# Performance work log

Hardware: AMD Instinct MI355X
Metric: run time of the kernel (lower is better)

The kernel has to match this reference:

```python
import jax, jax.numpy as jnp
import numpy as np
from jax import lax

TAU = 30.0  # softmax temperature


def setup_inputs() -> dict:
    key = jax.random.key(0)
    ks = jax.random.split(key, 6)
    N, Ci, Co, H, K, KW = 16, 64, 64, 256, 3, 4
    x = jax.random.normal(ks[0], (N, Ci, H, H), jnp.float32)
    # bank of KW candidate kernels: (Co, KW, Ci, K, K), kaiming-ish scale
    w_bank = jax.random.normal(ks[1], (Co, KW, Ci, K, K), jnp.float32) * (2.0 / (Co * K * K)) ** 0.5
    b_bank = jax.random.normal(ks[2], (Co, KW), jnp.float32) * 0.01
    # attention MLP (two 1x1 convs): Ci -> Ci//KW -> KW
    att_w1 = jax.random.normal(ks[3], (Ci // KW, Ci), jnp.float32) * (1.0 / Ci) ** 0.5
    att_b1 = jnp.zeros((Ci // KW,), jnp.float32)
    att_w2 = jax.random.normal(ks[4], (KW, Ci // KW), jnp.float32) * (KW / Ci) ** 0.5
    att_b2 = jnp.zeros((KW,), jnp.float32)
    return {"x": x, "w_bank": w_bank, "b_bank": b_bank,
            "att_w1": att_w1, "att_b1": att_b1, "att_w2": att_w2, "att_b2": att_b2}


def reference(x, w_bank, b_bank, att_w1, att_b1, att_w2, att_b2):
    # attention over weight banks: 1x1 conv -> ReLU -> 1x1 conv -> global avg pool -> softmax(/tau)
    h = jax.nn.relu(jnp.einsum('nchw,dc->ndhw', x, att_w1) + att_b1[None, :, None, None])
    logits = jnp.einsum('ndhw,ed->nehw', h, att_w2) + att_b2[None, :, None, None]
    pooled = jnp.mean(logits, axis=(2, 3))          # [N, KW] (avg_pool2d with kernel=H on square input)
    pi = jax.nn.softmax(pooled / TAU, axis=1)       # [N, KW]
    # per-sample aggregated kernels/biases
    w = jnp.einsum('okcij,nk->nocij', w_bank, pi)   # [N, Co, Ci, K, K]
    b = jnp.einsum('ok,nk->no', b_bank, pi)         # [N, Co]
    # per-sample conv (equivalent to the groups=N conv2d trick)
    def conv_one(xi, wi):
        return lax.conv_general_dilated(xi[None], wi, window_strides=(1, 1),
                                        padding=[(1, 1), (1, 1)],
                                        dimension_numbers=('NCHW', 'OIHW', 'NCHW'))[0]
    y = jax.vmap(conv_one)(x, w)                    # [N, Co, H, W]
    return y + b[:, :, None, None]
```

## Files before the change

### kernel.cpp

```cpp
#include <hip/hip_runtime.h>
#include <hip/hip_bf16.h>

typedef short short8 __attribute__((ext_vector_type(8)));
typedef float f32x4 __attribute__((ext_vector_type(4)));
typedef unsigned short ushort_t;

#define AS1 __attribute__((address_space(1)))
#define AS3 __attribute__((address_space(3)))

__device__ __forceinline__ ushort_t f2bf(float f) {
    unsigned u = __builtin_bit_cast(unsigned, f);
    unsigned r = (u + 0x7FFFu + ((u >> 16) & 1u)) >> 16;
    return (ushort_t)r;
}

__device__ __forceinline__ void gload_lds16(const void* g, void* l) {
    __builtin_amdgcn_global_load_lds((const AS1 unsigned*)g, (AS3 unsigned*)l, 16, 0, 0);
}

__global__ __launch_bounds__(256) void dc_k0_zeroborder(ushort_t* __restrict__ x_t)
{
    const int b = blockIdx.x, t = threadIdx.x;
    const int n = b >> 1, row = (b & 1) ? 257 : 0;
    short8 z = {0, 0, 0, 0, 0, 0, 0, 0};
    short8* p = reinterpret_cast<short8*>(x_t + (size_t)(n * 258 + row) * 258 * 64);
    for (int i = t; i < 2064; i += 256) p[i] = z;
}

__global__ __launch_bounds__(256) void dc_k1_stage_attn(
    const float* __restrict__ x, const float* __restrict__ w1,
    const float* __restrict__ b1, float* __restrict__ s_glob,
    ushort_t* __restrict__ x_t)
{
    __shared__ unsigned xt32[256 * 32];
    __shared__ ushort_t w1s[16 * 64];
    __shared__ float sacc[16];

    const int n = blockIdx.y, h = blockIdx.x, t = threadIdx.x;
    if (t < 16) sacc[t] = 0.f;
#pragma unroll
    for (int q = 0; q < 4; ++q) { int idx = q * 256 + t; w1s[idx] = f2bf(w1[idx]); }

    const float* xr = x + ((size_t)n * 64) * 65536 + (size_t)h * 256;
    const int sw = (t & 7) << 2;
    for (int cp = 0; cp < 32; ++cp) {
        float a = xr[(size_t)(2 * cp) * 65536 + t];
        float b = xr[(size_t)(2 * cp + 1) * 65536 + t];
        xt32[(t * 32 + cp) ^ sw] = (unsigned)f2bf(a) | ((unsigned)f2bf(b) << 16);
    }
    __syncthreads();

    const int lane = t & 63, wv = t >> 6, l15 = lane & 15, lg = lane >> 4;
    const short8* xt8 = reinterpret_cast<const short8*>(xt32);
    const short8* w18 = reinterpret_cast<const short8*>(w1s);

    short8 a0 = w18[l15 * 8 + lg];
    short8 a1 = w18[l15 * 8 + 4 + lg];
    float b1v[4];
#pragma unroll
    for (int r = 0; r < 4; ++r) b1v[r] = b1[lg * 4 + r];

    float rs[4] = {0.f, 0.f, 0.f, 0.f};
#pragma unroll
    for (int q = 0; q < 4; ++q) {
        int px = (wv * 4 + q) * 16 + l15;
        int pb = px * 8, ps = px & 7;
        short8 bb0 = xt8[pb + (lg ^ ps)];
        short8 bb1 = xt8[pb + ((4 + lg) ^ ps)];
        f32x4 hacc = {0.f, 0.f, 0.f, 0.f};
        hacc = __builtin_amdgcn_mfma_f32_16x16x32_bf16(a0, bb0, hacc, 0, 0, 0);
        hacc = __builtin_amdgcn_mfma_f32_16x16x32_bf16(a1, bb1, hacc, 0, 0, 0);
#pragma unroll
        for (int r = 0; r < 4; ++r) rs[r] += fmaxf(hacc[r] + b1v[r], 0.f);
    }
#pragma unroll
    for (int off = 1; off < 16; off <<= 1)
#pragma unroll
        for (int r = 0; r < 4; ++r) rs[r] += __shfl_xor(rs[r], off);
    if (l15 == 0) {
#pragma unroll
        for (int r = 0; r < 4; ++r) atomicAdd(&sacc[lg * 4 + r], rs[r]);
    }
    __syncthreads();
    if (t < 16) atomicAdd(&s_glob[n * 16 + t], sacc[t]);

    ushort_t* xo = x_t + (((size_t)n * 258 + h + 1) * 258 + 1) * 64;
    const int cb = t & 7, pxr = t >> 3;
#pragma unroll
    for (int rr = 0; rr < 8; ++rr) {
        int px = rr * 32 + pxr;
        short8 v = xt8[px * 8 + (cb ^ (px & 7))];
        *reinterpret_cast<short8*>(xo + (size_t)px * 64 + cb * 8) = v;
    }
    if (t < 16) {
        short8 z = {0, 0, 0, 0, 0, 0, 0, 0};
        size_t colbase = (((size_t)n * 258 + h + 1) * 258 + ((t < 8) ? 0 : 257)) * 64;
        reinterpret_cast<short8*>(x_t + colbase)[t & 7] = z;
    }
}

__global__ void dc_k2a_softmax_bias(
    const float* __restrict__ s_glob, const float* __restrict__ w2,
    const float* __restrict__ b2, const float* __restrict__ b_bank,
    float* __restrict__ pi, float* __restrict__ b_agg)
{
    __shared__ float piL[16][4];
    const int t = threadIdx.x;
    if (t < 16) {
        int n = t;
        float z[4];
#pragma unroll
        for (int e = 0; e < 4; ++e) {
            float p = 0.f;
            for (int d = 0; d < 16; ++d) p += w2[e * 16 + d] * s_glob[n * 16 + d];
            z[e] = (b2[e] + p * (1.f / 65536.f)) * (1.f / 30.f);
        }
        float m = fmaxf(fmaxf(z[0], z[1]), fmaxf(z[2], z[3]));
        float ex[4], sum = 0.f;
#pragma unroll
        for (int e = 0; e < 4; ++e) { ex[e] = expf(z[e] - m); sum += ex[e]; }
        float inv = 1.f / sum;
#pragma unroll
        for (int e = 0; e < 4; ++e) { float v = ex[e] * inv; pi[n * 4 + e] = v; piL[n][e] = v; }
    }
    __syncthreads();
    for (int r = 0; r < 16; ++r) {
        float v = 0.f;
#pragma unroll
        for (int kw = 0; kw < 4; ++kw) v += piL[r][kw] * b_bank[t * 4 + kw];
        b_agg[r * 64 + t] = v;
    }
}

__global__ void dc_k2b_aggw(const float* __restrict__ w_bank,
                            const float* __restrict__ pi,
                            ushort_t* __restrict__ A_frag)
{
    __shared__ float lw[2304];
    const int o = blockIdx.x, n = blockIdx.y, t = threadIdx.x;
    const float* wrow = w_bank + (size_t)o * 2304;
    for (int rr = 0; rr < 36; ++rr) lw[rr * 64 + t] = wrow[rr * 64 + t];
    float p0 = pi[n * 4 + 0], p1 = pi[n * 4 + 1], p2 = pi[n * 4 + 2], p3 = pi[n * 4 + 3];
    __syncthreads();
    const int c = t;
    const int cc = c >> 5, lg = (c >> 3) & 3, e = c & 7;
    const int mf = o >> 4, l15 = o & 15;
    ushort_t* base = A_frag + (size_t)n * 18 * 4 * 64 * 8;
#pragma unroll
    for (int ij = 0; ij < 9; ++ij) {
        float v = p0 * lw[0 * 576 + c * 9 + ij] + p1 * lw[1 * 576 + c * 9 + ij]
                + p2 * lw[2 * 576 + c * 9 + ij] + p3 * lw[3 * 576 + c * 9 + ij];
        int ks = ij * 2 + cc;
        base[(((ks * 4 + mf) * 64) + (lg * 16 + l15)) * 8 + e] = f2bf(v);
    }
}

__global__ __launch_bounds__(256, 1) void dc_k3_conv(
    const ushort_t* __restrict__ x_t, const ushort_t* __restrict__ A_frag,
    const float* __restrict__ b_agg, float* __restrict__ out)
{
    __shared__ char lds[73728 + 5 * 17408];
    char* ldsA = lds;
    char* ldsW = lds + 73728;

    int bid = blockIdx.x;
    int nb = (bid & 7) * 32 + (bid >> 3);
    const int n = nb >> 4;
    const int half = nb & 1;
    const int strip = (nb >> 1) & 7;
    const int h0 = strip * 32;
    const int w0 = half << 7;

    const int t = threadIdx.x, lane = t & 63, wv = t >> 6;
    const int l15 = lane & 15, lg = lane >> 4;
    const int pxl = wv * 32;

    const char* srcb = (const char*)x_t;
    const char* Asrc = (const char*)A_frag + (size_t)n * 73728;

    auto stage_row = [&](int rr, int slot) {
        size_t rowoff = ((size_t)(n * 258 + h0 + rr) * 258 + w0) * 128;
        char* dst = ldsW + slot * 17408;
        for (int k = wv; k < 17; k += 4) {
            unsigned q = k * 1024 + lane * 16;
            unsigned so = q ^ (((q >> 7) & 7) << 4);
            gload_lds16(srcb + rowoff + so, dst + k * 1024);
        }
    };

    for (int q = 0; q < 18; ++q) {
        int j = wv * 18 + q;
        gload_lds16(Asrc + j * 1024 + lane * 16, ldsA + j * 1024);
    }
    for (int r = 0; r < 4; ++r) stage_row(r, r);
    asm volatile("s_waitcnt vmcnt(0)" ::: "memory");
    __builtin_amdgcn_s_barrier();
    __builtin_amdgcn_sched_barrier(0);

    int boff[3][2][2];
#pragma unroll
    for (int kj = 0; kj < 3; ++kj)
#pragma unroll
        for (int cc = 0; cc < 2; ++cc)
#pragma unroll
            for (int nf = 0; nf < 2; ++nf) {
                int colL = pxl + nf * 16 + l15 + kj;
                boff[kj][cc][nf] = (colL * 128 + cc * 64 + lg * 16)
                                   ^ ((colL & 7) << 4);
            }
    const int aoff = lane * 16;

    const float* bn = b_agg + n * 64;
    float bv[4][4];
#pragma unroll
    for (int mf = 0; mf < 4; ++mf)
#pragma unroll
        for (int r = 0; r < 4; ++r) bv[mf][r] = bn[mf * 16 + lg * 4 + r];

#pragma unroll 1
    for (int j = 0; j < 16; ++j) {
        const int r0 = 2 * j;
        const int r4 = r0 + 4, r5 = r0 + 5;

        if (r4 <= 33) stage_row(r4, r4 % 5);
        __builtin_amdgcn_sched_barrier(0);

        const char* sb[4] = { ldsW + (r0 % 5) * 17408,
                              ldsW + ((r0 + 1) % 5) * 17408,
                              ldsW + ((r0 + 2) % 5) * 17408,
                              ldsW + ((r0 + 3) % 5) * 17408 };

        f32x4 acc[4][2][2] = {};
        short8 afb[2][4], bfb[2][2][2];

#pragma unroll
        for (int mf = 0; mf < 4; ++mf)
            afb[0][mf] = *reinterpret_cast<const short8*>(ldsA + mf * 1024 + aoff);
#pragma unroll
        for (int o = 0; o < 2; ++o)
#pragma unroll
            for (int nf = 0; nf < 2; ++nf)
                bfb[0][o][nf] = *reinterpret_cast<const short8*>(sb[o] + boff[0][0][nf]);

#pragma unroll
        for (int ks = 0; ks < 18; ++ks) {
            if (ks == 6) {
                __builtin_amdgcn_s_barrier();
                if (r5 <= 33) stage_row(r5, r0 % 5);
                __builtin_amdgcn_sched_barrier(0);
            }
            const int cur = ks & 1, nxt = cur ^ 1;
            if (ks < 17) {
                const int k1 = ks + 1;
                const int ki1 = k1 / 6, rem = k1 % 6;
                const int kj1 = rem >> 1, cc1 = rem & 1;
#pragma unroll
                for (int mf = 0; mf < 4; ++mf)
                    afb[nxt][mf] = *reinterpret_cast<const short8*>(
                        ldsA + (k1 * 4 + mf) * 1024 + aoff);
#pragma unroll
                for (int o = 0; o < 2; ++o)
#pragma unroll
                    for (int nf = 0; nf < 2; ++nf)
                        bfb[nxt][o][nf] = *reinterpret_cast<const short8*>(
                            sb[ki1 + o] + boff[kj1][cc1][nf]);
            }
#pragma unroll
            for (int mf = 0; mf < 4; ++mf)
#pragma unroll
                for (int nf = 0; nf < 2; ++nf)
#pragma unroll
                    for (int o = 0; o < 2; ++o)
                        acc[mf][nf][o] = __builtin_amdgcn_mfma_f32_16x16x32_bf16(
                            afb[cur][mf], bfb[cur][o][nf], acc[mf][nf][o], 0, 0, 0);
        }

#pragma unroll
        for (int o = 0; o < 2; ++o) {
            const int h = h0 + r0 + o;
#pragma unroll
            for (int mf = 0; mf < 4; ++mf)
#pragma unroll
                for (int nf = 0; nf < 2; ++nf) {
                    const int col = w0 + pxl + nf * 16 + l15;
#pragma unroll
                    for (int r = 0; r < 4; ++r)
                        out[((size_t)(n * 64 + mf * 16 + lg * 4 + r) << 16)
                            + (size_t)h * 256 + col] = acc[mf][nf][o][r] + bv[mf][r];
                }
        }
        __builtin_amdgcn_sched_barrier(0);
        asm volatile("s_waitcnt vmcnt(63)" ::: "memory");
        __builtin_amdgcn_s_barrier();
        __builtin_amdgcn_sched_barrier(0);
    }
}

extern "C" void kernel_launch(void* const* d_in, const int* in_sizes, int n_in,
                              void* d_out, int out_size, void* d_ws, size_t ws_size,
                              hipStream_t stream) {
    const float* x      = (const float*)d_in[0];
    const float* w_bank = (const float*)d_in[1];
    const float* b_bank = (const float*)d_in[2];
    const float* att_w1 = (const float*)d_in[3];
    const float* att_b1 = (const float*)d_in[4];
    const float* att_w2 = (const float*)d_in[5];
    const float* att_b2 = (const float*)d_in[6];
    float* out = (float*)d_out;

    char* ws = (char*)d_ws;
    float*    s_glob = (float*)ws;
    float*    pi     = (float*)(ws + 1024);
    float*    b_agg  = (float*)(ws + 2048);
    ushort_t* A_frag = (ushort_t*)(ws + 8192);
    ushort_t* x_t    = (ushort_t*)(ws + (2ull << 20));

    hipMemsetAsync(s_glob, 0, 16 * 16 * sizeof(float), stream);

    dc_k0_zeroborder<<<32, 256, 0, stream>>>(x_t);
    dc_k1_stage_attn<<<dim3(256, 16), 256, 0, stream>>>(x, att_w1, att_b1, s_glob, x_t);
    dc_k2a_softmax_bias<<<1, 64, 0, stream>>>(s_glob, att_w2, att_b2, b_bank, pi, b_agg);
    dc_k2b_aggw<<<dim3(64, 16), 64, 0, stream>>>(w_bank, pi, A_frag);
    dc_k3_conv<<<256, 256, 0, stream>>>(x_t, A_frag, b_agg, out);
}
```

Measured before the change: 195.6 us.

## Split conv work across eight waves per block and raise MFMA priority

Doubles the conv block to 512 threads (8 waves), with each wave covering 16 output columns instead of 32. Staging loops are respread over 8 waves and the vmcnt wait threshold is adjusted to match. This halves per-wave accumulators and B fragments, which is meant to hide LDS latency through more waves per CU. s_setprio is also raised around the MFMA sequence. The trade-off is that each B fragment feeds half as many MFMAs and each wave issues more A-fragment LDS reads per MFMA.

```diff
diff --git a/kernel.cpp b/kernel.cpp
--- a/kernel.cpp
+++ b/kernel.cpp
@@ -155,7 +155,7 @@
     }
 }
 
-__global__ __launch_bounds__(256, 1) void dc_k3_conv(
+__global__ __launch_bounds__(512, 1) void dc_k3_conv(
     const ushort_t* __restrict__ x_t, const ushort_t* __restrict__ A_frag,
     const float* __restrict__ b_agg, float* __restrict__ out)
 {
@@ -173,7 +173,7 @@
 
     const int t = threadIdx.x, lane = t & 63, wv = t >> 6;
     const int l15 = lane & 15, lg = lane >> 4;
-    const int pxl = wv * 32;
+    const int pxl = wv * 16;
 
     const char* srcb = (const char*)x_t;
     const char* Asrc = (const char*)A_frag + (size_t)n * 73728;
@@ -181,15 +181,15 @@
     auto stage_row = [&](int rr, int slot) {
         size_t rowoff = ((size_t)(n * 258 + h0 + rr) * 258 + w0) * 128;
         char* dst = ldsW + slot * 17408;
-        for (int k = wv; k < 17; k += 4) {
+        for (int k = wv; k < 17; k += 8) {
             unsigned q = k * 1024 + lane * 16;
             unsigned so = q ^ (((q >> 7) & 7) << 4);
             gload_lds16(srcb + rowoff + so, dst + k * 1024);
         }
     };
 
-    for (int q = 0; q < 18; ++q) {
-        int j = wv * 18 + q;
+    for (int q = 0; q < 9; ++q) {
+        int j = wv * 9 + q;
         gload_lds16(Asrc + j * 1024 + lane * 16, ldsA + j * 1024);
     }
     for (int r = 0; r < 4; ++r) stage_row(r, r);
@@ -197,17 +197,15 @@
     __builtin_amdgcn_s_barrier();
     __builtin_amdgcn_sched_barrier(0);
 
-    int boff[3][2][2];
+    int boff[3][2];
 #pragma unroll
     for (int kj = 0; kj < 3; ++kj)
 #pragma unroll
-        for (int cc = 0; cc < 2; ++cc)
-#pragma unroll
-            for (int nf = 0; nf < 2; ++nf) {
-                int colL = pxl + nf * 16 + l15 + kj;
-                boff[kj][cc][nf] = (colL * 128 + cc * 64 + lg * 16)
-                                   ^ ((colL & 7) << 4);
-            }
+        for (int cc = 0; cc < 2; ++cc) {
+            int colL = pxl + l15 + kj;
+            boff[kj][cc] = (colL * 128 + cc * 64 + lg * 16)
+                           ^ ((colL & 7) << 4);
+        }
     const int aoff = lane * 16;
 
     const float* bn = b_agg + n * 64;
@@ -230,17 +228,15 @@
                               ldsW + ((r0 + 2) % 5) * 17408,
                               ldsW + ((r0 + 3) % 5) * 17408 };
 
-        f32x4 acc[4][2][2] = {};
-        short8 afb[2][4], bfb[2][2][2];
+        f32x4 acc[4][2] = {};
+        short8 afb[2][4], bfb[2][2];
 
 #pragma unroll
         for (int mf = 0; mf < 4; ++mf)
             afb[0][mf] = *reinterpret_cast<const short8*>(ldsA + mf * 1024 + aoff);
 #pragma unroll
         for (int o = 0; o < 2; ++o)
-#pragma unroll
-            for (int nf = 0; nf < 2; ++nf)
-                bfb[0][o][nf] = *reinterpret_cast<const short8*>(sb[o] + boff[0][0][nf]);
+            bfb[0][o] = *reinterpret_cast<const short8*>(sb[o] + boff[0][0]);
 
 #pragma unroll
         for (int ks = 0; ks < 18; ++ks) {
@@ -260,37 +256,33 @@
                         ldsA + (k1 * 4 + mf) * 1024 + aoff);
 #pragma unroll
                 for (int o = 0; o < 2; ++o)
-#pragma unroll
-                    for (int nf = 0; nf < 2; ++nf)
-                        bfb[nxt][o][nf] = *reinterpret_cast<const short8*>(
-                            sb[ki1 + o] + boff[kj1][cc1][nf]);
+                    bfb[nxt][o] = *reinterpret_cast<const short8*>(
+                        sb[ki1 + o] + boff[kj1][cc1]);
             }
+            __builtin_amdgcn_s_setprio(1);
 #pragma unroll
             for (int mf = 0; mf < 4; ++mf)
 #pragma unroll
-                for (int nf = 0; nf < 2; ++nf)
-#pragma unroll
-                    for (int o = 0; o < 2; ++o)
-                        acc[mf][nf][o] = __builtin_amdgcn_mfma_f32_16x16x32_bf16(
-                            afb[cur][mf], bfb[cur][o][nf], acc[mf][nf][o], 0, 0, 0);
+                for (int o = 0; o < 2; ++o)
+                    acc[mf][o] = __builtin_amdgcn_mfma_f32_16x16x32_bf16(
+                        afb[cur][mf], bfb[cur][o], acc[mf][o], 0, 0, 0);
+            __builtin_amdgcn_s_setprio(0);
         }
 
 #pragma unroll
         for (int o = 0; o < 2; ++o) {
             const int h = h0 + r0 + o;
 #pragma unroll
-            for (int mf = 0; mf < 4; ++mf)
-#pragma unroll
-                for (int nf = 0; nf < 2; ++nf) {
-                    const int col = w0 + pxl + nf * 16 + l15;
-#pragma unroll
-                    for (int r = 0; r < 4; ++r)
-                        out[((size_t)(n * 64 + mf * 16 + lg * 4 + r) << 16)
-                            + (size_t)h * 256 + col] = acc[mf][nf][o][r] + bv[mf][r];
-                }
+            for (int mf = 0; mf < 4; ++mf) {
+                const int col = w0 + pxl + l15;
+#pragma unroll
+                for (int r = 0; r < 4; ++r)
+                    out[((size_t)(n * 64 + mf * 16 + lg * 4 + r) << 16)
+                        + (size_t)h * 256 + col] = acc[mf][o][r] + bv[mf][r];
+            }
         }
         __builtin_amdgcn_sched_barrier(0);
-        asm volatile("s_waitcnt vmcnt(63)" ::: "memory");
+        asm volatile("s_waitcnt vmcnt(31)" ::: "memory");
         __builtin_amdgcn_s_barrier();
         __builtin_amdgcn_sched_barrier(0);
     }
@@ -321,5 +313,5 @@
     dc_k1_stage_attn<<<dim3(256, 16), 256, 0, stream>>>(x, att_w1, att_b1, s_glob, x_t);
     dc_k2a_softmax_bias<<<1, 64, 0, stream>>>(s_glob, att_w2, att_b2, b_bank, pi, b_agg);
     dc_k2b_aggw<<<dim3(64, 16), 64, 0, stream>>>(w_bank, pi, A_frag);
-    dc_k3_conv<<<256, 256, 0, stream>>>(x_t, A_frag, b_agg, out);
-}
+    dc_k3_conv<<<256, 512, 0, stream>>>(x_t, A_frag, b_agg, out);
+}
```

Measured after the change: 190.9 us. 1.02x faster.
